# Optimization experiments

Measured on AMD Instinct MI355X. Metric: run time of the kernel, lower is better.

## Reference

```python
import jax, jax.numpy as jnp
import numpy as np

NUM_CLASSES = 40
EOS_COEF = 0.1
IGNORE = 255
W_CLASS, W_MASK, W_DICE = 2.0, 5.0, 5.0
EPS = 1e-8


def setup_inputs() -> dict:
    key = jax.random.key(0)
    k1, k2, k3, k4 = jax.random.split(key, 4)
    B, Q, H, W = 4, 100, 256, 256
    pred_logits = jax.random.normal(k1, (B, Q, NUM_CLASSES + 1), dtype=jnp.float32)
    pred_masks = jax.random.normal(k2, (B, Q, H, W), dtype=jnp.float32)
    targets = jax.random.randint(k3, (B, H, W), 0, NUM_CLASSES)
    ign = jax.random.uniform(k4, (B, H, W)) < 0.05
    targets = jnp.where(ign, IGNORE, targets).astype(jnp.int32)
    return {"pred_logits": pred_logits, "pred_masks": pred_masks, "targets": targets}


def reference(pred_logits, pred_masks, targets):
    B, Q, _ = pred_logits.shape
    C = NUM_CLASSES
    f32 = jnp.float32
    valid = targets != IGNORE                      # [B,H,W]
    tgt_safe = jnp.where(valid, targets, 0)        # in-range for indexing

    # ---- loss_labels: pixel->query assignment, per-query mode label ----
    # sigmoid is monotone, so argmax over queries of raw logits == argmax of sigmoid
    assign = jnp.argmax(pred_masks, axis=1)        # [B,H,W]
    b_idx = jnp.broadcast_to(jnp.arange(B)[:, None, None], targets.shape)
    # counts[b,q,c] = #valid pixels assigned to query q with label c
    counts = jnp.zeros((B, Q, C), f32).at[b_idx, assign, tgt_safe].add(valid.astype(f32))
    has_pix = counts.sum(-1) > 0                   # [B,Q]
    # mode = argmax of counts (ties -> smallest class, matching torch.mode)
    target_classes = jnp.where(has_pix, jnp.argmax(counts, axis=-1), C)  # [B,Q]

    logp = jax.nn.log_softmax(pred_logits, axis=-1)                      # [B,Q,C+1]
    nll = -jnp.take_along_axis(logp, target_classes[..., None], axis=-1)[..., 0]
    empty_weight = jnp.ones(C + 1, f32).at[-1].set(EOS_COEF)
    # ignore_index = num_classes in the CE over classes
    ce = jnp.where(target_classes != C, nll * empty_weight[target_classes], 0.0)
    p = jnp.exp(-ce)
    loss_ce = jnp.mean((1.0 - p) ** 2 * ce)

    # ---- loss_masks: per-pixel CE over queries + per-class dice ----
    logp_pix = jax.nn.log_softmax(pred_masks, axis=1)                    # [B,Q,H,W]
    nll_pix = -jnp.take_along_axis(logp_pix, tgt_safe[:, None], axis=1)[:, 0]  # [B,H,W]
    n_valid = valid.astype(f32).sum()
    ce_mask = jnp.sum(jnp.where(valid, nll_pix, 0.0)) / jnp.maximum(n_valid, 1.0)

    sig = jax.nn.sigmoid(pred_masks)                                     # [B,Q,H,W]
    tmask = (targets[:, None] == jnp.arange(C)[None, :, None, None]).astype(f32)  # [B,C,H,W]
    vm = valid[:, None].astype(f32)                                      # [B,1,H,W]
    inter = jnp.einsum('bqhw,bchw->bqc', sig, tmask * vm)                # numerator uses valid mask
    src_sum = sig.sum(axis=(2, 3))                                       # [B,Q]
    tsum = tmask.sum(axis=(2, 3))                                        # [B,C]
    dice = 2.0 * inter / (src_sum[:, :, None] + tsum[:, None, :] + EPS)  # [B,Q,C]
    present = tsum.sum(axis=0) > 0                                       # [C]
    dice_loss = jnp.sum(jnp.where(present, 1.0 - dice.mean(axis=(0, 1)), 0.0)) / C

    combined = W_MASK * ce_mask + W_DICE * dice_loss
    return W_CLASS * loss_ce + combined
```

## Files before the change

### kernel.cpp

```cpp
#include <hip/hip_runtime.h>
#include <hip/hip_bf16.h>

constexpr int B = 4, Q = 100, C = 40, Cp1 = 41, HW = 65536;
constexpr int NPIX = B * HW;

constexpr int ATHR = 256, APX = 2;
constexpr int ABLKS = NPIX / (ATHR * APX);
constexpr int ASLOT = HW / (ATHR * APX);
constexpr int QU = 5;

constexpr int BCH = 8;
constexpr int BCPX = HW / BCH;
constexpr int BIT = BCPX / (ATHR * 4);

constexpr int GRID = ABLKS + B * Q * BCH;

constexpr int WS_WORDS = 32562;

__global__ void kZ(unsigned* __restrict__ ws, int n) {
    int i = blockIdx.x * blockDim.x + threadIdx.x;
    for (; i < n; i += gridDim.x * blockDim.x) ws[i] = 0u;
}

__global__ __launch_bounds__(256, 4) void kBig(const float* __restrict__ masks,
                                               const int* __restrict__ targets,
                                               unsigned* __restrict__ counts,
                                               unsigned* __restrict__ tsum,
                                               float* __restrict__ ce_sum,
                                               unsigned* __restrict__ n_valid,
                                               float* __restrict__ inter,
                                               float* __restrict__ src_sum) {
    __shared__ float hist[C][ATHR];
    int tid = threadIdx.x;
    int blk = blockIdx.x;

    if (blk < ABLKS) {
        unsigned* ts_local = (unsigned*)&hist[0][0];
        float*    cred     = &hist[0][64];
        unsigned* vred     = (unsigned*)&hist[0][72];

        int b = blk / ASLOT;
        int hw = (blk % ASLOT) * (ATHR * APX) + tid * APX;
        const float* mp = masks + (size_t)b * Q * HW + hw;
        int2 tg = *(const int2*)(targets + (size_t)b * HW + hw);
        int tgs[2] = {tg.x, tg.y};

        float m[2] = {-INFINITY, -INFINITY}, s[2] = {0.f, 0.f}, xt[2] = {0.f, 0.f};
        int amax[2] = {0, 0};

        for (int qq = 0; qq < Q; qq += QU) {
            float2 vv[QU];
            #pragma unroll
            for (int u = 0; u < QU; ++u)
                vv[u] = *(const float2*)(mp + (size_t)(qq + u) * HW);
            #pragma unroll
            for (int u = 0; u < QU; ++u) {
                int q = qq + u;
                float v[2] = {vv[u].x, vv[u].y};
                #pragma unroll
                for (int j = 0; j < 2; ++j) {
                    s[j] += __expf(v[j]);
                    amax[j] = (v[j] > m[j]) ? q : amax[j];
                    m[j] = fmaxf(m[j], v[j]);
                    xt[j] = (q == tgs[j]) ? v[j] : xt[j];
                }
            }
        }

        if (tid < C) ts_local[tid] = 0u;
        __syncthreads();

        float ce = 0.f;
        unsigned nv = 0;
        #pragma unroll
        for (int j = 0; j < 2; ++j) {
            if (tgs[j] != 255) {
                ce += __logf(s[j]) - xt[j];
                nv++;
                atomicAdd(&counts[((size_t)b * Q + amax[j]) * C + tgs[j]], 1u);
                atomicAdd(&ts_local[tgs[j]], 1u);
            }
        }
        for (int off = 32; off; off >>= 1) {
            ce += __shfl_xor(ce, off);
            nv += __shfl_xor(nv, off);
        }
        int lane = tid & 63, wave = tid >> 6;
        if (lane == 0) { cred[wave] = ce; vred[wave] = nv; }
        __syncthreads();
        if (tid == 0) {
            atomicAdd(ce_sum, cred[0] + cred[1] + cred[2] + cred[3]);
            atomicAdd(n_valid, vred[0] + vred[1] + vred[2] + vred[3]);
        }
        if (tid < C) {
            unsigned t = ts_local[tid];
            if (t) atomicAdd(&tsum[b * C + tid], t);
        }
    } else {
        int r = blk - ABLKS;
        int bq = r >> 3;
        int chunk = r & 7;
        int b = bq / Q;
        const float* mp = masks + (size_t)bq * HW + chunk * BCPX;
        const int* tp = targets + (size_t)b * HW + chunk * BCPX;

        #pragma unroll
        for (int c = 0; c < C; ++c) hist[c][tid] = 0.f;

        float sacc = 0.f;
        #pragma unroll 2
        for (int it = 0; it < BIT; ++it) {
            int off = it * (ATHR * 4) + tid * 4;
            float4 x = *(const float4*)(mp + off);
            int4 tg = *(const int4*)(tp + off);
            float xs[4] = {x.x, x.y, x.z, x.w};
            int cs[4] = {tg.x, tg.y, tg.z, tg.w};
            #pragma unroll
            for (int j = 0; j < 4; ++j) {
                float sig = 1.f / (1.f + __expf(-xs[j]));
                sacc += sig;
                if ((unsigned)cs[j] < (unsigned)C) hist[cs[j]][tid] += sig;
            }
        }

        for (int off = 32; off; off >>= 1) sacc += __shfl_xor(sacc, off);
        int lane = tid & 63, wave = tid >> 6;
        if (lane == 0) atomicAdd(&src_sum[bq], sacc);

        __syncthreads();
        for (int c = wave * 10; c < wave * 10 + 10; ++c) {
            float h = hist[c][lane] + hist[c][lane + 64] + hist[c][lane + 128] + hist[c][lane + 192];
            for (int off = 32; off; off >>= 1) h += __shfl_xor(h, off);
            if (lane == 0) atomicAdd(&inter[(size_t)bq * C + c], h);
        }
    }
}

__global__ __launch_bounds__(512) void kC(const float* __restrict__ logits,
                                          const unsigned* __restrict__ counts,
                                          const unsigned* __restrict__ tsum,
                                          const float* __restrict__ inter,
                                          const float* __restrict__ src_sum,
                                          const float* __restrict__ ce_sum,
                                          const unsigned* __restrict__ n_valid,
                                          float* __restrict__ out) {
    int tid = threadIdx.x;
    __shared__ float dice_sum[C];
    __shared__ float wred[8];
    __shared__ float s_lce;
    if (tid < C) dice_sum[tid] = 0.f;

    float ce_acc = 0.f;
    for (int i = tid; i < B * Q; i += 512) {
        const unsigned* cnt = counts + (size_t)i * C;
        unsigned best = 0;
        int tc = C;
        #pragma unroll
        for (int c = 0; c < C; ++c) {
            unsigned v = cnt[c];
            if (v > best) { best = v; tc = c; }
        }
        if (tc != C) {
            const float* lg = logits + (size_t)i * Cp1;
            float mm = -INFINITY, xt = 0.f;
            #pragma unroll
            for (int c = 0; c < Cp1; ++c) {
                float v = lg[c];
                mm = fmaxf(mm, v);
                if (c == tc) xt = v;
            }
            float ss = 0.f;
            #pragma unroll
            for (int c = 0; c < Cp1; ++c) ss += __expf(lg[c] - mm);
            float nll = mm + __logf(ss) - xt;
            float p = __expf(-nll);
            float om = 1.f - p;
            ce_acc += om * om * nll;
        }
    }
    for (int off = 32; off; off >>= 1) ce_acc += __shfl_xor(ce_acc, off);
    if ((tid & 63) == 0) wred[tid >> 6] = ce_acc;
    __syncthreads();
    if (tid == 0) {
        float t = 0.f;
        for (int w = 0; w < 8; ++w) t += wred[w];
        s_lce = t;
    }

    for (int i = tid; i < B * Q * C; i += 512) {
        int bq = i / C, c = i - bq * C;
        float denom = src_sum[bq] + (float)tsum[(bq / Q) * C + c] + 1e-8f;
        atomicAdd(&dice_sum[c], 2.f * inter[i] / denom);
    }
    __syncthreads();

    if (tid == 0) {
        float dl = 0.f;
        for (int c = 0; c < C; ++c) {
            unsigned ts = tsum[c] + tsum[C + c] + tsum[2 * C + c] + tsum[3 * C + c];
            if (ts > 0) dl += 1.f - dice_sum[c] * (1.f / (B * Q));
        }
        dl *= (1.f / C);
        float ce_mask = ce_sum[0] / fmaxf((float)n_valid[0], 1.f);
        float lce = s_lce * (1.f / (B * Q));
        out[0] = 2.f * lce + 5.f * ce_mask + 5.f * dl;
    }
}

extern "C" void kernel_launch(void* const* d_in, const int* in_sizes, int n_in,
                              void* d_out, int out_size, void* d_ws, size_t ws_size,
                              hipStream_t stream) {
    const float* logits  = (const float*)d_in[0];
    const float* masks   = (const float*)d_in[1];
    const int*   targets = (const int*)d_in[2];
    float* out = (float*)d_out;

    unsigned* ws      = (unsigned*)d_ws;
    unsigned* counts  = ws;
    unsigned* tsum    = ws + 16000;
    float*    inter   = (float*)(ws + 16160);
    float*    src_sum = (float*)(ws + 32160);
    float*    ce_sum  = (float*)(ws + 32560);
    unsigned* n_valid = ws + 32561;

    kZ<<<64, 256, 0, stream>>>(ws, WS_WORDS);
    kBig<<<GRID, ATHR, 0, stream>>>(masks, targets, counts, tsum, ce_sum, n_valid,
                                    inter, src_sum);
    kC<<<1, 512, 0, stream>>>(logits, counts, tsum, inter, src_sum, ce_sum, n_valid, out);
}
```

Baseline: 226.7 us.

## Replace LDS per-class histogram with register accumulators in dice blocks

The dice/intersection blocks now keep the 40 per-class sums in registers and update them with branchless compare-select adds, replacing the 40KB shared-memory histogram with its data-dependent LDS read-modify-write. The per-class sums are reduced across each wave with shuffles and then combined across waves in a small shared buffer. Shared memory drops to 640 bytes, which frees occupancy, and the sigmoid uses a fast reciprocal. In exchange every pixel now costs 160 compare/select adds, so the kernel does much more ALU work, and the launch-bounds occupancy hint is removed.

```diff
diff --git a/kernel.cpp b/kernel.cpp
--- a/kernel.cpp
+++ b/kernel.cpp
@@ -22,22 +22,23 @@
     for (; i < n; i += gridDim.x * blockDim.x) ws[i] = 0u;
 }
 
-__global__ __launch_bounds__(256, 4) void kBig(const float* __restrict__ masks,
-                                               const int* __restrict__ targets,
-                                               unsigned* __restrict__ counts,
-                                               unsigned* __restrict__ tsum,
-                                               float* __restrict__ ce_sum,
-                                               unsigned* __restrict__ n_valid,
-                                               float* __restrict__ inter,
-                                               float* __restrict__ src_sum) {
-    __shared__ float hist[C][ATHR];
+__global__ __launch_bounds__(256) void kBig(const float* __restrict__ masks,
+                                            const int* __restrict__ targets,
+                                            unsigned* __restrict__ counts,
+                                            unsigned* __restrict__ tsum,
+                                            float* __restrict__ ce_sum,
+                                            unsigned* __restrict__ n_valid,
+                                            float* __restrict__ inter,
+                                            float* __restrict__ src_sum) {
+    __shared__ float smem[4 * C];
     int tid = threadIdx.x;
     int blk = blockIdx.x;
+    int lane = tid & 63, wave = tid >> 6;
 
     if (blk < ABLKS) {
-        unsigned* ts_local = (unsigned*)&hist[0][0];
-        float*    cred     = &hist[0][64];
-        unsigned* vred     = (unsigned*)&hist[0][72];
+        unsigned* ts_local = (unsigned*)&smem[0];
+        float*    cred     = &smem[64];
+        unsigned* vred     = (unsigned*)&smem[72];
 
         int b = blk / ASLOT;
         int hw = (blk % ASLOT) * (ATHR * APX) + tid * APX;
@@ -85,7 +86,6 @@
             ce += __shfl_xor(ce, off);
             nv += __shfl_xor(nv, off);
         }
-        int lane = tid & 63, wave = tid >> 6;
         if (lane == 0) { cred[wave] = ce; vred[wave] = nv; }
         __syncthreads();
         if (tid == 0) {
@@ -104,34 +104,47 @@
         const float* mp = masks + (size_t)bq * HW + chunk * BCPX;
         const int* tp = targets + (size_t)b * HW + chunk * BCPX;
 
-        #pragma unroll
-        for (int c = 0; c < C; ++c) hist[c][tid] = 0.f;
+        float acc[C];
+        #pragma unroll
+        for (int k = 0; k < C; ++k) acc[k] = 0.f;
 
         float sacc = 0.f;
-        #pragma unroll 2
         for (int it = 0; it < BIT; ++it) {
             int off = it * (ATHR * 4) + tid * 4;
             float4 x = *(const float4*)(mp + off);
             int4 tg = *(const int4*)(tp + off);
             float xs[4] = {x.x, x.y, x.z, x.w};
             int cs[4] = {tg.x, tg.y, tg.z, tg.w};
+            float sg[4];
             #pragma unroll
             for (int j = 0; j < 4; ++j) {
-                float sig = 1.f / (1.f + __expf(-xs[j]));
-                sacc += sig;
-                if ((unsigned)cs[j] < (unsigned)C) hist[cs[j]][tid] += sig;
-            }
-        }
-
-        for (int off = 32; off; off >>= 1) sacc += __shfl_xor(sacc, off);
-        int lane = tid & 63, wave = tid >> 6;
-        if (lane == 0) atomicAdd(&src_sum[bq], sacc);
-
+                sg[j] = __builtin_amdgcn_rcpf(1.f + __expf(-xs[j]));
+                sacc += sg[j];
+            }
+            #pragma unroll
+            for (int k = 0; k < C; ++k) {
+                float add = 0.f;
+                #pragma unroll
+                for (int j = 0; j < 4; ++j)
+                    add += (cs[j] == k) ? sg[j] : 0.f;
+                acc[k] += add;
+            }
+        }
+
+        float ss = sacc;
+        for (int off = 32; off; off >>= 1) ss += __shfl_xor(ss, off);
+        if (lane == 0) atomicAdd(&src_sum[bq], ss);
+
+        #pragma unroll
+        for (int k = 0; k < C; ++k) {
+            float a = acc[k];
+            for (int off = 32; off; off >>= 1) a += __shfl_xor(a, off);
+            if (lane == 0) smem[wave * C + k] = a;
+        }
         __syncthreads();
-        for (int c = wave * 10; c < wave * 10 + 10; ++c) {
-            float h = hist[c][lane] + hist[c][lane + 64] + hist[c][lane + 128] + hist[c][lane + 192];
-            for (int off = 32; off; off >>= 1) h += __shfl_xor(h, off);
-            if (lane == 0) atomicAdd(&inter[(size_t)bq * C + c], h);
+        if (tid < C) {
+            float t = smem[tid] + smem[C + tid] + smem[2 * C + tid] + smem[3 * C + tid];
+            atomicAdd(&inter[(size_t)bq * C + tid], t);
         }
     }
 }
```

Result: slower. 265.8 us (+17.2%).
